# Performance work log

Measured on AMD Instinct MI355X. Metric: run time of the kernel, lower is better.

Reference implementation:

```python
import jax, jax.numpy as jnp
import numpy as np

N = 200000   # num atoms (nodes)
E = 400000   # one-way edges; symmetrized to 2E inside forward
H = 256      # hidden_dim == hidden_feats
LN_EPS = 1e-5


def setup_inputs() -> dict:
    key = jax.random.key(0)
    ks = jax.random.split(key, 48)
    def p(i, shape, s=0.05):
        return jax.random.normal(ks[i], shape, dtype=jnp.float32) * s
    inp = {
        'atom_inputs': jax.random.randint(ks[0], (N, 7), 0, 2),
        'src': jax.random.randint(ks[1], (E,), 0, N),
        'dst': jax.random.randint(ks[2], (E,), 0, N),
        # AtomEmbedding tables
        'emb_element': p(3, (100, 64)),
        'emb_degree': p(4, (7, 4)),
        'emb_valence': p(5, (7, 4)),
        'emb_charge': p(6, (8, 4)),
        'emb_aromatic': p(7, (2, 4)),
        'emb_hybrid': p(8, (6, 4)),
        'emb_hydrogen': p(9, (5, 4)),
        # linear_0: 88 -> H
        'W0': p(10, (88, H)), 'b0': jnp.zeros((H,), jnp.float32),
        # linear_1: H -> H
        'W1': p(11, (H, H)), 'b1': jnp.zeros((H,), jnp.float32),
    }
    # 4 GINEConv layers: node-MLP weight Wn/bn, edge Linear(1,H) weight We/be,
    # followed by LayerNorm gamma g / beta bt
    for i in range(4):
        inp[f'Wn{i}'] = p(12 + 4 * i, (H, H))
        inp[f'bn{i}'] = jnp.zeros((H,), jnp.float32)
        inp[f'We{i}'] = p(13 + 4 * i, (H,))
        inp[f'be{i}'] = jnp.zeros((H,), jnp.float32)
        inp[f'g{i}'] = jnp.ones((H,), jnp.float32)
        inp[f'bt{i}'] = jnp.zeros((H,), jnp.float32)
    return inp


def _layernorm(x, g, b):
    m = jnp.mean(x, axis=-1, keepdims=True)
    v = jnp.mean(jnp.square(x - m), axis=-1, keepdims=True)
    return (x - m) / jnp.sqrt(v + LN_EPS) * g + b


def reference(atom_inputs, src, dst,
              emb_element, emb_degree, emb_valence, emb_charge,
              emb_aromatic, emb_hybrid, emb_hydrogen,
              W0, b0, W1, b1,
              Wn0, bn0, We0, be0, g0, bt0,
              Wn1, bn1, We1, be1, g1, bt1,
              Wn2, bn2, We2, be2, g2, bt2,
              Wn3, bn3, We3, be3, g3, bt3):
    # --- AtomEmbedding: 7 lookups, concat -> [N, 88]
    feats = jnp.concatenate([
        emb_element[atom_inputs[:, 0]],
        emb_degree[atom_inputs[:, 1]],
        emb_valence[atom_inputs[:, 2] + 1],
        emb_charge[atom_inputs[:, 3]],
        emb_aromatic[atom_inputs[:, 4]],
        emb_hybrid[atom_inputs[:, 5]],
        emb_hydrogen[atom_inputs[:, 6]],
    ], axis=-1)
    h = feats @ W0 + b0  # [N, H]
    n = h.shape[0]

    # symmetrize edges: src||dst -> dst||src
    s = jnp.concatenate([src, dst])
    d = jnp.concatenate([dst, src])

    def gine(x, Wn, bn, We, be):
        # edge_attr is all-ones [2E,1]; Linear(1,H) applied to ones is the
        # constant vector We + be broadcast over edges.
        c = We + be                                   # [H]
        msg = jax.nn.relu(x[s] + c)                   # [2E, H] gather + add
        agg = jax.ops.segment_sum(msg, d, num_segments=n)  # scatter-sum
        return (x + agg) @ Wn + bn                    # eps=0: (1+eps)*x + agg

    h = _layernorm(gine(h, Wn0, bn0, We0, be0), g0, bt0)
    h = _layernorm(gine(h, Wn1, bn1, We1, be1), g1, bt1)
    h = _layernorm(gine(h, Wn2, bn2, We2, be2), g2, bt2)
    h = _layernorm(gine(h, Wn3, bn3, We3, be3), g3, bt3)
    return h @ W1 + b1
```

## Files before the change

kernel.cpp:

```cpp
#include <hip/hip_runtime.h>

#define HDIM 256

typedef __attribute__((ext_vector_type(8))) short short8;
typedef __attribute__((ext_vector_type(4))) float f32x4;

typedef const __attribute__((address_space(1))) unsigned int* gas_ptr;
typedef __attribute__((address_space(3))) unsigned int* las_ptr;

__device__ __forceinline__ unsigned short f2bf(float f) {
    unsigned int u = __float_as_uint(f);
    u += 0x7FFF + ((u >> 16) & 1);
    return (unsigned short)(u >> 16);
}
__device__ __forceinline__ float bf2f(unsigned short u) {
    return __uint_as_float(((unsigned int)u) << 16);
}


__global__ void k_zero_int(int* p, int n) {
    int i = blockIdx.x * blockDim.x + threadIdx.x;
    if (i < n) p[i] = 0;
}

__global__ void k_hist(const int* __restrict__ src, const int* __restrict__ dst,
                       int E, int* __restrict__ deg) {
    int e = blockIdx.x * blockDim.x + threadIdx.x;
    if (e >= E) return;
    atomicAdd(&deg[dst[e]], 1);
    atomicAdd(&deg[src[e]], 1);
}

__global__ void k_scan_partial(const int* __restrict__ deg, int* __restrict__ rp,
                               int* __restrict__ bsum, int n) {
    __shared__ int sd[256];
    int t = threadIdx.x;
    int base = blockIdx.x * 1024 + t * 4;
    int v[4]; int tsum = 0;
    #pragma unroll
    for (int k = 0; k < 4; k++) { v[k] = (base + k < n) ? deg[base + k] : 0; tsum += v[k]; }
    sd[t] = tsum; __syncthreads();
    for (int off = 1; off < 256; off <<= 1) {
        int x = (t >= off) ? sd[t - off] : 0;
        __syncthreads();
        sd[t] += x;
        __syncthreads();
    }
    int run = sd[t] - tsum;
    if (t == 255) bsum[blockIdx.x] = sd[255];
    #pragma unroll
    for (int k = 0; k < 4; k++) { if (base + k < n) rp[base + k] = run; run += v[k]; }
}

__global__ void k_scan_bsum(int* __restrict__ bsum, int nb) {
    __shared__ int sd[256];
    int t = threadIdx.x;
    int base = t * 4;
    int v[4]; int tsum = 0;
    #pragma unroll
    for (int k = 0; k < 4; k++) { v[k] = (base + k < nb) ? bsum[base + k] : 0; tsum += v[k]; }
    sd[t] = tsum; __syncthreads();
    for (int off = 1; off < 256; off <<= 1) {
        int x = (t >= off) ? sd[t - off] : 0;
        __syncthreads();
        sd[t] += x;
        __syncthreads();
    }
    int run = sd[t] - tsum;
    #pragma unroll
    for (int k = 0; k < 4; k++) { if (base + k < nb) bsum[base + k] = run; run += v[k]; }
}

__global__ void k_scan_add(int* __restrict__ rp, int* __restrict__ cursor,
                           const int* __restrict__ bsum, int n, int twoE) {
    int i = blockIdx.x * blockDim.x + threadIdx.x;
    if (i < n) {
        int v = rp[i] + bsum[i >> 10];
        rp[i] = v;
        cursor[i] = v;
    }
    if (i == 0) rp[n] = twoE;
}

__global__ void k_fill(const int* __restrict__ src, const int* __restrict__ dst,
                       int E, int* __restrict__ cursor, int* __restrict__ col) {
    int e = blockIdx.x * blockDim.x + threadIdx.x;
    if (e >= E) return;
    int s = src[e], d = dst[e];
    int p = atomicAdd(&cursor[d], 1); col[p] = s;
    int q = atomicAdd(&cursor[s], 1); col[q] = d;
}


__global__ void k_prep_w(const float* __restrict__ W, unsigned short* __restrict__ Wt) {
    int k = blockIdx.x, nn = threadIdx.x;
    Wt[nn * 256 + k] = f2bf(W[k * 256 + nn]);
}

__global__ void k_prep_w0(const float* __restrict__ W0, unsigned short* __restrict__ Wt0) {
    int k = blockIdx.x, nn = threadIdx.x;
    Wt0[nn * 96 + k] = (k < 88) ? f2bf(W0[k * 256 + nn]) : 0;
}


__global__ __launch_bounds__(256) void k_embed0(
    const int* __restrict__ atom,
    const float* __restrict__ eE, const float* __restrict__ eD,
    const float* __restrict__ eV, const float* __restrict__ eC,
    const float* __restrict__ eA, const float* __restrict__ eH,
    const float* __restrict__ eHy,
    const unsigned short* __restrict__ Wt0, const float* __restrict__ b0,
    unsigned short* __restrict__ x, int n) {
    __shared__ __align__(128) unsigned short As[64 * 256];
    int t = threadIdx.x;
    size_t node0 = (size_t)blockIdx.x * 64;

    {
        int row = t >> 2;
        int ks  = (t & 3) * 24;
        size_t node = node0 + row;
        int a0 = 0, a1 = 0, a2 = 0, a3 = 0, a4 = 0, a5 = 0, a6 = 0;
        bool ok = node < (size_t)n;
        if (ok) {
            const int* a = atom + node * 7;
            a0 = a[0]; a1 = a[1]; a2 = a[2]; a3 = a[3]; a4 = a[4]; a5 = a[5]; a6 = a[6];
        }
        #pragma unroll
        for (int kk = 0; kk < 24; kk++) {
            int k = ks + kk;
            float val = 0.f;
            if (ok) {
                if (k < 64)       val = eE[a0 * 64 + k];
                else if (k < 68)  val = eD[a1 * 4 + (k - 64)];
                else if (k < 72)  val = eV[(a2 + 1) * 4 + (k - 68)];
                else if (k < 76)  val = eC[a3 * 4 + (k - 72)];
                else if (k < 80)  val = eA[a4 * 4 + (k - 76)];
                else if (k < 84)  val = eH[a5 * 4 + (k - 80)];
                else if (k < 88)  val = eHy[a6 * 4 + (k - 84)];
            }
            int boff = (k * 2) ^ ((row & 7) << 4);
            *(unsigned short*)((char*)As + row * 256 + boff) = f2bf(val);
        }
    }
    __syncthreads();

    int w  = t >> 6;
    int l  = t & 63;
    int lr = l & 15;
    int lk = l >> 4;

    f32x4 acc[4][4];
    #pragma unroll
    for (int rg = 0; rg < 4; rg++)
        #pragma unroll
        for (int cg = 0; cg < 4; cg++)
            acc[rg][cg] = (f32x4){0.f, 0.f, 0.f, 0.f};

    #pragma unroll
    for (int kt = 0; kt < 3; kt++) {
        int kbyte = kt * 64 + lk * 16;
        short8 a[4], bf[4];
        #pragma unroll
        for (int rg = 0; rg < 4; rg++) {
            int row = rg * 16 + lr;
            a[rg] = *(const short8*)((const char*)As + row * 256 + (kbyte ^ ((row & 7) << 4)));
        }
        #pragma unroll
        for (int cg = 0; cg < 4; cg++) {
            int coln = w * 64 + cg * 16 + lr;
            bf[cg] = *(const short8*)((const char*)Wt0 + coln * 192 + kbyte);
        }
        #pragma unroll
        for (int rg = 0; rg < 4; rg++)
            #pragma unroll
            for (int cg = 0; cg < 4; cg++)
                acc[rg][cg] = __builtin_amdgcn_mfma_f32_16x16x32_bf16(a[rg], bf[cg], acc[rg][cg], 0, 0, 0);
    }

    float bcol[4];
    #pragma unroll
    for (int cg = 0; cg < 4; cg++) bcol[cg] = b0[w * 64 + cg * 16 + lr];

    __syncthreads();
    #pragma unroll
    for (int rg = 0; rg < 4; rg++)
        #pragma unroll
        for (int j = 0; j < 4; j++) {
            int row = rg * 16 + lk * 4 + j;
            #pragma unroll
            for (int cg = 0; cg < 4; cg++) {
                int colI = w * 64 + cg * 16 + lr;
                int byte = row * 512 + ((((colI >> 2) << 3) ^ ((row & 7) << 4)) + (colI & 3) * 2);
                *(unsigned short*)((char*)As + byte) = f2bf(acc[rg][cg][j] + bcol[cg]);
            }
        }
    __syncthreads();
    ushort4* xo = (ushort4*)(x + node0 * HDIM);
    #pragma unroll
    for (int i = 0; i < 16; i++) {
        int g4 = i * 256 + t;
        int row = g4 >> 6, c4 = g4 & 63;
        if (node0 + row < (size_t)n)
            xo[g4] = *(ushort4*)((char*)As + row * 512 + ((c4 << 3) ^ ((row & 7) << 4)));
    }
}


__global__ __launch_bounds__(512) void k_gine(
    const unsigned short* __restrict__ x, const int* __restrict__ rp,
    const int* __restrict__ col, const float* __restrict__ We,
    const float* __restrict__ be, const unsigned short* __restrict__ Wt,
    const float* __restrict__ b, const float* __restrict__ g,
    const float* __restrict__ bt, unsigned short* __restrict__ xout, int n) {
    __shared__ __align__(128) unsigned short As[64 * 256];
    __shared__ float psum[8][64], psq[8][64];
    __shared__ float mean_s[64], inv_s[64];

    int t = threadIdx.x;
    int wid = t >> 6;
    int l = t & 63;
    int h = l >> 5;
    int j = l & 31;
    size_t node0 = (size_t)blockIdx.x * 64;

    {
        int hh = wid * 2 + h;
        const short8* x8 = (const short8*)x;
        float c[8];
        {
            float4 w0 = ((const float4*)We)[2 * j], w1 = ((const float4*)We)[2 * j + 1];
            float4 e0 = ((const float4*)be)[2 * j], e1 = ((const float4*)be)[2 * j + 1];
            c[0] = w0.x + e0.x; c[1] = w0.y + e0.y; c[2] = w0.z + e0.z; c[3] = w0.w + e0.w;
            c[4] = w1.x + e1.x; c[5] = w1.y + e1.y; c[6] = w1.z + e1.z; c[7] = w1.w + e1.w;
        }
        for (int q = 0; q < 4; q++) {
            int row = hh * 4 + q;
            size_t node = node0 + row;
            bool ok = node < (size_t)n;
            int nd = ok ? (int)node : 0;
            int p0 = rp[nd], p1 = rp[nd + 1];
            int deg = ok ? (p1 - p0) : 0;

            float acc[8];
            short8 s = x8[(size_t)nd * 32 + j];
            #pragma unroll
            for (int k = 0; k < 8; k++) acc[k] = ok ? bf2f((unsigned short)s[k]) : 0.f;

            for (int bb = 0; bb < deg; bb += 32) {
                int m = deg - bb; if (m > 32) m = 32;
                int idx = (j < m) ? col[p0 + bb + j] : 0;
                int e = 0;
                for (; e + 2 <= m; e += 2) {
                    int s0 = __shfl(idx, (h << 5) + e, 64);
                    int s1 = __shfl(idx, (h << 5) + e + 1, 64);
                    short8 u0 = x8[(size_t)s0 * 32 + j];
                    short8 u1 = x8[(size_t)s1 * 32 + j];
                    #pragma unroll
                    for (int k = 0; k < 8; k++) acc[k] += fmaxf(bf2f((unsigned short)u0[k]) + c[k], 0.f);
                    #pragma unroll
                    for (int k = 0; k < 8; k++) acc[k] += fmaxf(bf2f((unsigned short)u1[k]) + c[k], 0.f);
                }
                if (e < m) {
                    int s0 = __shfl(idx, (h << 5) + e, 64);
                    short8 u0 = x8[(size_t)s0 * 32 + j];
                    #pragma unroll
                    for (int k = 0; k < 8; k++) acc[k] += fmaxf(bf2f((unsigned short)u0[k]) + c[k], 0.f);
                }
            }

            short8 o;
            #pragma unroll
            for (int k = 0; k < 8; k++) o[k] = (short)f2bf(acc[k]);
            *(short8*)((char*)As + row * 512 + ((j ^ (row & 7)) << 4)) = o;
        }
    }
    __syncthreads();

    int lr = l & 15;
    int lk = l >> 4;

    f32x4 acc[2][4];
    #pragma unroll
    for (int fg = 0; fg < 2; fg++)
        #pragma unroll
        for (int ng = 0; ng < 4; ng++)
            acc[fg][ng] = (f32x4){0.f, 0.f, 0.f, 0.f};

    #pragma unroll
    for (int kt = 0; kt < 8; kt++) {
        int kbyte = kt * 64 + lk * 16;
        short8 a[2], bfr[4];
        #pragma unroll
        for (int fg = 0; fg < 2; fg++) {
            int feat = wid * 32 + fg * 16 + lr;
            a[fg] = *(const short8*)((const char*)Wt + feat * 512 + kbyte);
        }
        #pragma unroll
        for (int ng = 0; ng < 4; ng++) {
            int row = ng * 16 + lr;
            bfr[ng] = *(const short8*)((const char*)As + row * 512 + (kbyte ^ ((row & 7) << 4)));
        }
        #pragma unroll
        for (int fg = 0; fg < 2; fg++)
            #pragma unroll
            for (int ng = 0; ng < 4; ng++)
                acc[fg][ng] = __builtin_amdgcn_mfma_f32_16x16x32_bf16(a[fg], bfr[ng], acc[fg][ng], 0, 0, 0);
    }

    #pragma unroll
    for (int fg = 0; fg < 2; fg++) {
        float4 bv = *(const float4*)&b[wid * 32 + fg * 16 + 4 * lk];
        #pragma unroll
        for (int ng = 0; ng < 4; ng++) {
            acc[fg][ng][0] += bv.x; acc[fg][ng][1] += bv.y;
            acc[fg][ng][2] += bv.z; acc[fg][ng][3] += bv.w;
        }
    }

    float sv[4], sq[4];
    #pragma unroll
    for (int ng = 0; ng < 4; ng++) {
        float s = 0.f, q = 0.f;
        #pragma unroll
        for (int fg = 0; fg < 2; fg++)
            #pragma unroll
            for (int jj = 0; jj < 4; jj++) {
                float v = acc[fg][ng][jj];
                s += v; q += v * v;
            }
        sv[ng] = s; sq[ng] = q;
    }
    #pragma unroll
    for (int ng = 0; ng < 4; ng++) {
        sv[ng] += __shfl_xor(sv[ng], 16, 64);
        sq[ng] += __shfl_xor(sq[ng], 16, 64);
        sv[ng] += __shfl_xor(sv[ng], 32, 64);
        sq[ng] += __shfl_xor(sq[ng], 32, 64);
    }
    if (lk == 0) {
        #pragma unroll
        for (int ng = 0; ng < 4; ng++) {
            psum[wid][ng * 16 + lr] = sv[ng];
            psq[wid][ng * 16 + lr]  = sq[ng];
        }
    }
    __syncthreads();
    if (t < 64) {
        float s = 0.f, q = 0.f;
        #pragma unroll
        for (int wv = 0; wv < 8; wv++) { s += psum[wv][t]; q += psq[wv][t]; }
        float m = s * (1.f / 256.f);
        float var = q * (1.f / 256.f) - m * m;
        mean_s[t] = m;
        inv_s[t]  = rsqrtf(var + 1e-5f);
    }
    __syncthreads();

    #pragma unroll
    for (int fg = 0; fg < 2; fg++) {
        int fbase = wid * 32 + fg * 16 + 4 * lk;
        float4 gv  = *(const float4*)&g[fbase];
        float4 btv = *(const float4*)&bt[fbase];
        #pragma unroll
        for (int ng = 0; ng < 4; ng++) {
            int row = ng * 16 + lr;
            float m = mean_s[row];
            float inv = inv_s[row];
            ushort4 h4;
            h4.x = f2bf((acc[fg][ng][0] - m) * inv * gv.x + btv.x);
            h4.y = f2bf((acc[fg][ng][1] - m) * inv * gv.y + btv.y);
            h4.z = f2bf((acc[fg][ng][2] - m) * inv * gv.z + btv.z);
            h4.w = f2bf((acc[fg][ng][3] - m) * inv * gv.w + btv.w);
            int byte = row * 512 + ((fbase * 2) ^ ((row & 7) << 4));
            *(ushort4*)((char*)As + byte) = h4;
        }
    }
    __syncthreads();
    #pragma unroll
    for (int i = 0; i < 4; i++) {
        int g16 = i * 512 + t;
        int row = g16 >> 5, ch = g16 & 31;
        if (node0 + row < (size_t)n) {
            short8 v = *(const short8*)((const char*)As + row * 512 + ((ch ^ (row & 7)) << 4));
            ((short8*)xout)[(node0 + row) * 32 + ch] = v;
        }
    }
}


__global__ __launch_bounds__(256) void k_gemm_final(
    const unsigned short* __restrict__ zin, const unsigned short* __restrict__ Wt,
    const float* __restrict__ b, float* __restrict__ xout, int n) {
    __shared__ __align__(128) unsigned short As[64 * 256];

    int t = threadIdx.x;
    int w = t >> 6;
    int l = t & 63;
    size_t node0 = (size_t)blockIdx.x * 64;

    if (node0 + 64 <= (size_t)n) {
        const char* ztile = (const char*)(zin + node0 * HDIM);
        #pragma unroll
        for (int it = 0; it < 8; it++) {
            int ldsbase = w * 8192 + it * 1024;
            int row = (ldsbase >> 9) + (l >> 5);
            int chunk = (l & 31) * 16;
            const char* src = ztile + row * 512 + (chunk ^ ((row & 7) << 4));
            __builtin_amdgcn_global_load_lds((gas_ptr)src,
                                             (las_ptr)((char*)As + ldsbase),
                                             16, 0, 0);
        }
    } else {
        const ushort4* zr = (const ushort4*)(zin + node0 * HDIM);
        #pragma unroll
        for (int i = 0; i < 16; i++) {
            int g4 = i * 256 + t;
            int row = g4 >> 6, c4 = g4 & 63;
            ushort4 v = make_ushort4(0, 0, 0, 0);
            if (node0 + row < (size_t)n) v = zr[g4];
            *(ushort4*)((char*)As + row * 512 + ((c4 << 3) ^ ((row & 7) << 4))) = v;
        }
    }
    __syncthreads();

    int lr = l & 15;
    int lk = l >> 4;

    f32x4 acc[4][4];
    #pragma unroll
    for (int rg = 0; rg < 4; rg++)
        #pragma unroll
        for (int cg = 0; cg < 4; cg++)
            acc[rg][cg] = (f32x4){0.f, 0.f, 0.f, 0.f};

    #pragma unroll
    for (int kt = 0; kt < 8; kt++) {
        int kbyte = kt * 64 + lk * 16;
        short8 a[4], bf[4];
        #pragma unroll
        for (int rg = 0; rg < 4; rg++) {
            int row = rg * 16 + lr;
            a[rg] = *(const short8*)((const char*)As + row * 512 + (kbyte ^ ((row & 7) << 4)));
        }
        #pragma unroll
        for (int cg = 0; cg < 4; cg++) {
            int coln = w * 64 + cg * 16 + lr;
            bf[cg] = *(const short8*)((const char*)Wt + coln * 512 + kbyte);
        }
        #pragma unroll
        for (int rg = 0; rg < 4; rg++)
            #pragma unroll
            for (int cg = 0; cg < 4; cg++)
                acc[rg][cg] = __builtin_amdgcn_mfma_f32_16x16x32_bf16(a[rg], bf[cg], acc[rg][cg], 0, 0, 0);
    }

    float bcol[4];
    #pragma unroll
    for (int cg = 0; cg < 4; cg++) bcol[cg] = b[w * 64 + cg * 16 + lr];
    #pragma unroll
    for (int rg = 0; rg < 4; rg++)
        #pragma unroll
        for (int j = 0; j < 4; j++) {
            int row = rg * 16 + lk * 4 + j;
            size_t node = node0 + row;
            if (node < (size_t)n) {
                #pragma unroll
                for (int cg = 0; cg < 4; cg++)
                    xout[node * HDIM + w * 64 + cg * 16 + lr] = acc[rg][cg][j] + bcol[cg];
            }
        }
}


extern "C" void kernel_launch(void* const* d_in, const int* in_sizes, int n_in,
                              void* d_out, int out_size, void* d_ws, size_t ws_size,
                              hipStream_t stream) {
    const int*   atom = (const int*)d_in[0];
    const int*   src  = (const int*)d_in[1];
    const int*   dst  = (const int*)d_in[2];
    const float* eE   = (const float*)d_in[3];
    const float* eD   = (const float*)d_in[4];
    const float* eV   = (const float*)d_in[5];
    const float* eC   = (const float*)d_in[6];
    const float* eA   = (const float*)d_in[7];
    const float* eH   = (const float*)d_in[8];
    const float* eHy  = (const float*)d_in[9];
    const float* W0   = (const float*)d_in[10];
    const float* b0   = (const float*)d_in[11];
    const float* W1   = (const float*)d_in[12];
    const float* b1   = (const float*)d_in[13];

    const int N = in_sizes[0] / 7;
    const int E = in_sizes[1];
    const int twoE = 2 * E;

    unsigned short* xb = (unsigned short*)d_ws;
    unsigned short* z  = xb + (size_t)N * HDIM;
    int*   rp      = (int*)(z + (size_t)N * HDIM);
    int*   cursor  = rp + (N + 1);
    int*   deg     = cursor + N;
    int*   col     = deg + N;
    int*   bsum    = col + twoE;
    uintptr_t pw = (uintptr_t)(bsum + 1024);
    pw = (pw + 255) & ~(uintptr_t)255;
    unsigned short* Wt  = (unsigned short*)pw;
    unsigned short* Wt0 = Wt + (size_t)5 * 65536;

    const int nb = (N + 1023) / 1024;

    k_zero_int<<<(N + 255) / 256, 256, 0, stream>>>(deg, N);
    k_hist<<<(E + 255) / 256, 256, 0, stream>>>(src, dst, E, deg);
    k_scan_partial<<<nb, 256, 0, stream>>>(deg, rp, bsum, N);
    k_scan_bsum<<<1, 256, 0, stream>>>(bsum, nb);
    k_scan_add<<<(N + 255) / 256, 256, 0, stream>>>(rp, cursor, bsum, N, twoE);
    k_fill<<<(E + 255) / 256, 256, 0, stream>>>(src, dst, E, cursor, col);

    for (int L = 0; L < 4; L++) {
        const float* Wn = (const float*)d_in[14 + 6 * L + 0];
        k_prep_w<<<256, 256, 0, stream>>>(Wn, Wt + (size_t)L * 65536);
    }
    k_prep_w<<<256, 256, 0, stream>>>(W1, Wt + (size_t)4 * 65536);
    k_prep_w0<<<96, 256, 0, stream>>>(W0, Wt0);

    const int nblk64 = (N + 63) / 64;

    k_embed0<<<nblk64, 256, 0, stream>>>(atom, eE, eD, eV, eC, eA, eH, eHy,
                                         Wt0, b0, xb, N);

    unsigned short* cur = xb;
    unsigned short* nxt = z;
    for (int L = 0; L < 4; L++) {
        const float* bn = (const float*)d_in[14 + 6 * L + 1];
        const float* We = (const float*)d_in[14 + 6 * L + 2];
        const float* be = (const float*)d_in[14 + 6 * L + 3];
        const float* gg = (const float*)d_in[14 + 6 * L + 4];
        const float* bt = (const float*)d_in[14 + 6 * L + 5];
        k_gine<<<nblk64, 512, 0, stream>>>(cur, rp, col, We, be,
                                           Wt + (size_t)L * 65536, bn, gg, bt, nxt, N);
        unsigned short* tmp = cur; cur = nxt; nxt = tmp;
    }

    k_gemm_final<<<nblk64, 256, 0, stream>>>(cur, Wt + (size_t)4 * 65536,
                                             b1, (float*)d_out, N);
}
```

Measured before the change: 794.0 us.

## Interleave two nodes' edge gathers and write LayerNorm output directly to global

```diff
diff --git a/kernel.cpp b/kernel.cpp
--- a/kernel.cpp
+++ b/kernel.cpp
@@ -15,6 +15,12 @@
 }
 __device__ __forceinline__ float bf2f(unsigned short u) {
     return __uint_as_float(((unsigned int)u) << 16);
+}
+
+__device__ __forceinline__ void acc_edge(float (&acc)[8], const float (&c)[8], short8 u) {
+    #pragma unroll
+    for (int k = 0; k < 8; k++)
+        acc[k] += fmaxf(bf2f((unsigned short)u[k]) + c[k], 0.f);
 }
 
 
@@ -225,6 +231,7 @@
 
     {
         int hh = wid * 2 + h;
+        int row0 = hh * 4;
         const short8* x8 = (const short8*)x;
         float c[8];
         {
@@ -233,45 +240,102 @@
             c[0] = w0.x + e0.x; c[1] = w0.y + e0.y; c[2] = w0.z + e0.z; c[3] = w0.w + e0.w;
             c[4] = w1.x + e1.x; c[5] = w1.y + e1.y; c[6] = w1.z + e1.z; c[7] = w1.w + e1.w;
         }
-        for (int q = 0; q < 4; q++) {
-            int row = hh * 4 + q;
-            size_t node = node0 + row;
-            bool ok = node < (size_t)n;
-            int nd = ok ? (int)node : 0;
-            int p0 = rp[nd], p1 = rp[nd + 1];
-            int deg = ok ? (p1 - p0) : 0;
-
-            float acc[8];
-            short8 s = x8[(size_t)nd * 32 + j];
+
+        int off = h << 5;
+        int base = (int)node0 + row0;
+
+        int rpv = 0;
+        if (j < 5) {
+            int bi = base + j;
+            if (bi > n) bi = n;
+            rpv = rp[bi];
+        }
+        int p0 = __shfl(rpv, off + 0, 64);
+        int p1 = __shfl(rpv, off + 1, 64);
+        int p2 = __shfl(rpv, off + 2, 64);
+        int p3 = __shfl(rpv, off + 3, 64);
+        int p4 = __shfl(rpv, off + 4, 64);
+
+        int total = p4 - p0;
+        int idxr = (j < total) ? col[p0 + j] : 0;
+
+        #pragma unroll
+        for (int pass = 0; pass < 2; pass++) {
+            int rA = row0 + pass * 2;
+            int qa = (pass == 0) ? p0 : p2;
+            int qb = (pass == 0) ? p1 : p3;
+            int qc = (pass == 0) ? p2 : p4;
+            int d0 = qb - qa, d1 = qc - qb;
+            int oa = qa - p0, ob = qb - p0;
+
+            float acc0[8], acc1[8];
+            {
+                size_t nA = node0 + rA, nB = node0 + rA + 1;
+                bool ok0 = nA < (size_t)n, ok1 = nB < (size_t)n;
+                short8 s0 = x8[(ok0 ? nA : 0) * 32 + j];
+                short8 s1 = x8[(ok1 ? nB : 0) * 32 + j];
+                #pragma unroll
+                for (int k = 0; k < 8; k++) {
+                    acc0[k] = ok0 ? bf2f((unsigned short)s0[k]) : 0.f;
+                    acc1[k] = ok1 ? bf2f((unsigned short)s1[k]) : 0.f;
+                }
+            }
+
+            if (qc - p0 <= 32) {
+                int e0 = 0, e1 = 0;
+                int n2 = (d0 < d1) ? d0 : d1;
+                for (; e0 + 2 <= n2; e0 += 2, e1 += 2) {
+                    int i0 = __shfl(idxr, off + oa + e0, 64);
+                    int i1 = __shfl(idxr, off + oa + e0 + 1, 64);
+                    int i2 = __shfl(idxr, off + ob + e1, 64);
+                    int i3 = __shfl(idxr, off + ob + e1 + 1, 64);
+                    short8 u0 = x8[(size_t)i0 * 32 + j];
+                    short8 u1 = x8[(size_t)i1 * 32 + j];
+                    short8 u2 = x8[(size_t)i2 * 32 + j];
+                    short8 u3 = x8[(size_t)i3 * 32 + j];
+                    acc_edge(acc0, c, u0); acc_edge(acc0, c, u1);
+                    acc_edge(acc1, c, u2); acc_edge(acc1, c, u3);
+                }
+                if (e0 < n2) {
+                    int i0 = __shfl(idxr, off + oa + e0, 64);
+                    int i2 = __shfl(idxr, off + ob + e1, 64);
+                    short8 u0 = x8[(size_t)i0 * 32 + j];
+                    short8 u2 = x8[(size_t)i2 * 32 + j];
+                    acc_edge(acc0, c, u0); acc_edge(acc1, c, u2);
+                    e0++; e1++;
+                }
+                for (; e0 < d0; e0++) {
+                    int i0 = __shfl(idxr, off + oa + e0, 64);
+                    short8 u0 = x8[(size_t)i0 * 32 + j];
+                    acc_edge(acc0, c, u0);
+                }
+                for (; e1 < d1; e1++) {
+                    int i2 = __shfl(idxr, off + ob + e1, 64);
+                    short8 u2 = x8[(size_t)i2 * 32 + j];
+                    acc_edge(acc1, c, u2);
+                }
+            } else {
+                for (int e = 0; e < d0; e++) {
+                    int s = col[qa + e];
+                    short8 u = x8[(size_t)s * 32 + j];
+                    acc_edge(acc0, c, u);
+                }
+                for (int e = 0; e < d1; e++) {
+                    int s = col[qb + e];
+                    short8 u = x8[(size_t)s * 32 + j];
+                    acc_edge(acc1, c, u);
+                }
+            }
+
+            short8 o0, o1;
             #pragma unroll
-            for (int k = 0; k < 8; k++) acc[k] = ok ? bf2f((unsigned short)s[k]) : 0.f;
-
-            for (int bb = 0; bb < deg; bb += 32) {
-                int m = deg - bb; if (m > 32) m = 32;
-                int idx = (j < m) ? col[p0 + bb + j] : 0;
-                int e = 0;
-                for (; e + 2 <= m; e += 2) {
-                    int s0 = __shfl(idx, (h << 5) + e, 64);
-                    int s1 = __shfl(idx, (h << 5) + e + 1, 64);
-                    short8 u0 = x8[(size_t)s0 * 32 + j];
-                    short8 u1 = x8[(size_t)s1 * 32 + j];
-                    #pragma unroll
-                    for (int k = 0; k < 8; k++) acc[k] += fmaxf(bf2f((unsigned short)u0[k]) + c[k], 0.f);
-                    #pragma unroll
-                    for (int k = 0; k < 8; k++) acc[k] += fmaxf(bf2f((unsigned short)u1[k]) + c[k], 0.f);
-                }
-                if (e < m) {
-                    int s0 = __shfl(idx, (h << 5) + e, 64);
-                    short8 u0 = x8[(size_t)s0 * 32 + j];
-                    #pragma unroll
-                    for (int k = 0; k < 8; k++) acc[k] += fmaxf(bf2f((unsigned short)u0[k]) + c[k], 0.f);
-                }
-            }
-
-            short8 o;
-            #pragma unroll
-            for (int k = 0; k < 8; k++) o[k] = (short)f2bf(acc[k]);
-            *(short8*)((char*)As + row * 512 + ((j ^ (row & 7)) << 4)) = o;
+            for (int k = 0; k < 8; k++) {
+                o0[k] = (short)f2bf(acc0[k]);
+                o1[k] = (short)f2bf(acc1[k]);
+            }
+            int r1 = rA + 1;
+            *(short8*)((char*)As + rA * 512 + ((j ^ (rA & 7)) << 4)) = o0;
+            *(short8*)((char*)As + r1 * 512 + ((j ^ (r1 & 7)) << 4)) = o1;
         }
     }
     __syncthreads();
@@ -364,25 +428,17 @@
         #pragma unroll
         for (int ng = 0; ng < 4; ng++) {
             int row = ng * 16 + lr;
-            float m = mean_s[row];
-            float inv = inv_s[row];
-            ushort4 h4;
-            h4.x = f2bf((acc[fg][ng][0] - m) * inv * gv.x + btv.x);
-            h4.y = f2bf((acc[fg][ng][1] - m) * inv * gv.y + btv.y);
-            h4.z = f2bf((acc[fg][ng][2] - m) * inv * gv.z + btv.z);
-            h4.w = f2bf((acc[fg][ng][3] - m) * inv * gv.w + btv.w);
-            int byte = row * 512 + ((fbase * 2) ^ ((row & 7) << 4));
-            *(ushort4*)((char*)As + byte) = h4;
-        }
-    }
-    __syncthreads();
-    #pragma unroll
-    for (int i = 0; i < 4; i++) {
-        int g16 = i * 512 + t;
-        int row = g16 >> 5, ch = g16 & 31;
-        if (node0 + row < (size_t)n) {
-            short8 v = *(const short8*)((const char*)As + row * 512 + ((ch ^ (row & 7)) << 4));
-            ((short8*)xout)[(node0 + row) * 32 + ch] = v;
+            size_t node = node0 + row;
+            if (node < (size_t)n) {
+                float m = mean_s[row];
+                float inv = inv_s[row];
+                ushort4 h4;
+                h4.x = f2bf((acc[fg][ng][0] - m) * inv * gv.x + btv.x);
+                h4.y = f2bf((acc[fg][ng][1] - m) * inv * gv.y + btv.y);
+                h4.z = f2bf((acc[fg][ng][2] - m) * inv * gv.z + btv.z);
+                h4.w = f2bf((acc[fg][ng][3] - m) * inv * gv.w + btv.w);
+                *(ushort4*)(xout + node * HDIM + fbase) = h4;
+            }
         }
     }
 }
```

Result: slower. 861.2 us (+8.5%).
